# Kernel optimization log

Hardware: AMD Instinct MI355X
Metric: run time of the kernel (lower is better)

Reference implementation:

```python
import jax, jax.numpy as jnp
import numpy as np

EMB_DIM = 1024
B, K, N = 16, 512, 2048


def setup_inputs() -> dict:
    key0 = jax.random.key(0)
    k1, k2, k3, k4 = jax.random.split(key0, 4)
    query = jax.random.normal(k1, (K, EMB_DIM), dtype=jnp.float32)
    key = jax.random.normal(k2, (B, N, EMB_DIM), dtype=jnp.float32)
    # parameter W [emb_dim, emb_dim]; scale like kaiming-ish init
    W = jax.random.normal(k3, (EMB_DIM, EMB_DIM), dtype=jnp.float32) / np.sqrt(EMB_DIM)
    att_mask = jax.random.randint(k4, (B, K, N), 0, 2) > 0
    return {"query": query, "key": key, "W": W, "att_mask": att_mask}


def reference(query, key, W, att_mask):
    # 2D query / 3D key branch of SimpleConcatAttention, dim=-1
    d = query.shape[-1]
    # q @ W / sqrt(d): [K, d] (broadcast over batch instead of tiling)
    qW = (query @ W) / jnp.sqrt(jnp.asarray(d, query.dtype))
    # scores [b, K, N] = qW @ key^T
    att = jnp.einsum("kd,bnd->bkn", qW, key)
    att = jnp.where(att_mask, att, -jnp.inf)
    att = jax.nn.softmax(att, axis=-1)
    # out [b, K, d] = att @ key
    out = jnp.einsum("bkn,bnd->bkd", att, key)
    return out, att
```

## Files before the change

### kernel.cpp

```cpp
#include <hip/hip_runtime.h>


typedef float  f32x4  __attribute__((ext_vector_type(4)));
typedef short  bf16x8 __attribute__((ext_vector_type(8)));
typedef _Float16 f16x8 __attribute__((ext_vector_type(8)));
typedef unsigned short u16;
typedef unsigned short u16x8 __attribute__((ext_vector_type(8)));
typedef unsigned short u16x4 __attribute__((ext_vector_type(4)));

__device__ __forceinline__ void split2h(float x, u16& hi, u16& lo)
{
    _Float16 h = (_Float16)x;
    _Float16 l = (_Float16)(x - (float)h);
    hi = __builtin_bit_cast(u16, h);
    lo = __builtin_bit_cast(u16, l);
}

__device__ __forceinline__ void split2(float x, u16& hi, u16& lo)
{
    unsigned u = __float_as_uint(x);
    hi = (u16)(u >> 16);
    float hf = __uint_as_float(u & 0xFFFF0000u);
    float lf = x - hf;
    lo = (u16)(__float_as_uint(lf) >> 16);
}

__device__ __forceinline__ void async_cp16(const void* g, void* l)
{
    __builtin_amdgcn_global_load_lds(
        (const __attribute__((address_space(1))) unsigned int*)g,
        (__attribute__((address_space(3))) unsigned int*)l, 16, 0, 0);
}

template<int NMFMA, int BK>
__global__ __launch_bounds__(256, 2) void gemm_nt_f16(
    const u16* __restrict__ Ah, const u16* __restrict__ Al,
    const u16* __restrict__ Bh, const u16* __restrict__ Bl,
    float* __restrict__ C,
    int Kd, long sA, long sB, long sC, int ldc, float scale)
{
    constexpr int NPL = (NMFMA == 3) ? 4 : (NMFMA == 2) ? 3 : 2;
    constexpr int PS  = 128 * BK;
    constexpr int NCH = PS / 512;
    __shared__ __attribute__((aligned(16))) u16 lds[NPL * PS];
    u16* Ahs = lds;
    u16* Bhs = lds + PS;
    u16* Als = (NMFMA >= 2) ? lds + 2 * PS : nullptr;
    u16* Bls = (NMFMA == 3) ? lds + 3 * PS : nullptr;

    const int tid  = threadIdx.x;
    const int lane = tid & 63;
    const int wid  = tid >> 6;
    const int wm   = wid >> 1, wn = wid & 1;
    const int fr   = lane & 15;
    const int fq   = lane >> 4;

    const int m0 = blockIdx.y * 128, n0 = blockIdx.x * 128;
    const u16* Ag  = Ah + (long)blockIdx.z * sA + (long)m0 * Kd;
    const u16* Bg  = Bh + (long)blockIdx.z * sB + (long)n0 * Kd;
    const u16* Ag2 = (NMFMA >= 2) ? Al + (long)blockIdx.z * sA + (long)m0 * Kd : nullptr;
    const u16* Bg2 = (NMFMA == 3) ? Bl + (long)blockIdx.z * sB + (long)n0 * Kd : nullptr;

    f32x4 acc[4][4];
#pragma unroll
    for (int i = 0; i < 4; i++)
#pragma unroll
        for (int j = 0; j < 4; j++) acc[i][j] = (f32x4){0.f, 0.f, 0.f, 0.f};

    for (int k0 = 0; k0 < Kd; k0 += BK) {
        __syncthreads();
#pragma unroll
        for (int i = 0; i < NCH / 4; i++) {
            const int q   = wid * (NCH / 4) + i;
            const int p   = q * 512 + lane * 8;
            const int r   = p / BK;
            const int oct = (p & (BK - 1)) >> 3;
            const long go = (long)r * Kd + k0 + ((oct ^ (r & 7)) << 3);
            async_cp16(Ag + go, Ahs + q * 512);
            async_cp16(Bg + go, Bhs + q * 512);
            if constexpr (NMFMA >= 2) async_cp16(Ag2 + go, Als + q * 512);
            if constexpr (NMFMA == 3) async_cp16(Bg2 + go, Bls + q * 512);
        }
        __syncthreads();

#pragma unroll
        for (int ks = 0; ks < BK / 32; ks++) {
            const int cl = fq + ks * 4;
            f16x8 ah[4], bh[4], al[4], bl[4];
#pragma unroll
            for (int i = 0; i < 4; i++) {
                const int ra = wm * 64 + i * 16 + fr;
                const int oa = ra * BK + ((cl ^ (ra & 7)) << 3);
                ah[i] = *(const f16x8*)&Ahs[oa];
                if constexpr (NMFMA >= 2) al[i] = *(const f16x8*)&Als[oa];
                const int rb = wn * 64 + i * 16 + fr;
                const int ob = rb * BK + ((cl ^ (rb & 7)) << 3);
                bh[i] = *(const f16x8*)&Bhs[ob];
                if constexpr (NMFMA == 3) bl[i] = *(const f16x8*)&Bls[ob];
            }
#pragma unroll
            for (int i = 0; i < 4; i++)
#pragma unroll
                for (int j = 0; j < 4; j++) {
                    acc[i][j] = __builtin_amdgcn_mfma_f32_16x16x32_f16(ah[i], bh[j], acc[i][j], 0, 0, 0);
                    if constexpr (NMFMA == 3)
                        acc[i][j] = __builtin_amdgcn_mfma_f32_16x16x32_f16(ah[i], bl[j], acc[i][j], 0, 0, 0);
                    if constexpr (NMFMA >= 2)
                        acc[i][j] = __builtin_amdgcn_mfma_f32_16x16x32_f16(al[i], bh[j], acc[i][j], 0, 0, 0);
                }
        }
    }

    float* Cg = C + (long)blockIdx.z * sC + (long)(m0 + wm * 64) * ldc + (n0 + wn * 64);
    const int r4 = fq * 4;
#pragma unroll
    for (int i = 0; i < 4; i++)
#pragma unroll
        for (int j = 0; j < 4; j++) {
            float* cp = Cg + (long)(i * 16 + r4) * ldc + j * 16 + fr;
#pragma unroll
            for (int q = 0; q < 4; q++)
                cp[(long)q * ldc] = acc[i][j][q] * scale;
        }
}

__global__ __launch_bounds__(256) void prep_all(
    const float* __restrict__ query, const float* __restrict__ W,
    const float* __restrict__ key,
    u16* __restrict__ qW_h, u16* __restrict__ qW_l,
    u16* __restrict__ key_h, u16* __restrict__ keyT)
{
    constexpr int LDg = 72;
    __shared__ __attribute__((aligned(16))) u16 sm[4 * 64 * LDg];
    const int tid = threadIdx.x;

    if (blockIdx.x >= 128) {
        u16* t = sm;
        const int idx2 = (int)blockIdx.x - 128;
        const int bx = idx2 & 15, by = (idx2 >> 4) & 31, bz = idx2 >> 9;
        const long zin = (long)bz * 2048 * 1024;
        const int n0 = by * 64, d0 = bx * 64;
#pragma unroll
        for (int j = 0; j < 2; j++) {
            const int idx = tid + j * 256;
            const int row = idx >> 3;
            const int col = (idx & 7) * 8;
            const long g = zin + (long)(n0 + row) * 1024 + d0 + col;
            f32x4 v0 = *(const f32x4*)(key + g);
            f32x4 v1 = *(const f32x4*)(key + g + 4);
            u16x8 h;
#pragma unroll
            for (int e = 0; e < 4; e++) {
                _Float16 a = (_Float16)v0[e];
                _Float16 b = (_Float16)v1[e];
                h[e]     = __builtin_bit_cast(u16, a);
                h[4 + e] = __builtin_bit_cast(u16, b);
            }
            *(u16x8*)(key_h + g) = h;
#pragma unroll
            for (int e = 0; e < 8; e++) t[(col + e) * 65 + row] = h[e];
        }
        __syncthreads();
        const long zT = (long)bz * 1024 * 2048;
#pragma unroll
        for (int j = 0; j < 4; j++) {
            const int idx = tid + j * 256;
            const int dr = idx >> 4;
            const int nc = (idx & 15) * 4;
            u16x4 o = {t[dr * 65 + nc], t[dr * 65 + nc + 1],
                       t[dr * 65 + nc + 2], t[dr * 65 + nc + 3]};
            *(u16x4*)(keyT + zT + (long)(d0 + dr) * 2048 + n0 + nc) = o;
        }
        return;
    }

    u16* As_h = sm;
    u16* As_l = sm + 64 * LDg;
    u16* Bs_h = sm + 2 * 64 * LDg;
    u16* Bs_l = sm + 3 * 64 * LDg;

    const int lane = tid & 63, wid = tid >> 6;
    const int wm = wid >> 1, wn = wid & 1;
    const int lr = lane & 15, fq = lane >> 4;
    const int m0 = ((int)blockIdx.x >> 4) * 64;
    const int n0 = ((int)blockIdx.x & 15) * 64;
    const float* Ag = query + (long)m0 * 1024;
    const float* Bg = W + n0;

    __builtin_amdgcn_s_setprio(1);

    f32x4 acc[2][2];
#pragma unroll
    for (int i = 0; i < 2; i++)
#pragma unroll
        for (int j = 0; j < 2; j++) acc[i][j] = (f32x4){0.f, 0.f, 0.f, 0.f};

    for (int k0 = 0; k0 < 1024; k0 += 64) {
        __syncthreads();
        {
            const int row = tid >> 2, kb = (tid & 3) * 16;
            const float* src = Ag + (long)row * 1024 + k0 + kb;
            f32x4 v0 = *(const f32x4*)src;
            f32x4 v1 = *(const f32x4*)(src + 4);
            f32x4 v2 = *(const f32x4*)(src + 8);
            f32x4 v3 = *(const f32x4*)(src + 12);
            u16x8 h0, h1, l0, l1;
#pragma unroll
            for (int e = 0; e < 4; e++) {
                u16 hh, ll;
                split2h(v0[e], hh, ll); h0[e] = hh;     l0[e] = ll;
                split2h(v1[e], hh, ll); h0[4 + e] = hh; l0[4 + e] = ll;
                split2h(v2[e], hh, ll); h1[e] = hh;     l1[e] = ll;
                split2h(v3[e], hh, ll); h1[4 + e] = hh; l1[4 + e] = ll;
            }
            *(u16x8*)&As_h[row * LDg + kb]     = h0;
            *(u16x8*)&As_h[row * LDg + kb + 8] = h1;
            *(u16x8*)&As_l[row * LDg + kb]     = l0;
            *(u16x8*)&As_l[row * LDg + kb + 8] = l1;
        }
        {
            const int n = lane;
            u16x8 h0, h1, l0, l1;
#pragma unroll
            for (int kk = 0; kk < 8; kk++) {
                float x0 = Bg[(long)(k0 + wid * 16 + kk) * 1024 + n];
                float x1 = Bg[(long)(k0 + wid * 16 + 8 + kk) * 1024 + n];
                u16 hh, ll;
                split2h(x0, hh, ll); h0[kk] = hh; l0[kk] = ll;
                split2h(x1, hh, ll); h1[kk] = hh; l1[kk] = ll;
            }
            *(u16x8*)&Bs_h[n * LDg + wid * 16]     = h0;
            *(u16x8*)&Bs_h[n * LDg + wid * 16 + 8] = h1;
            *(u16x8*)&Bs_l[n * LDg + wid * 16]     = l0;
            *(u16x8*)&Bs_l[n * LDg + wid * 16 + 8] = l1;
        }
        __syncthreads();

#pragma unroll
        for (int ks = 0; ks < 2; ks++) {
            f16x8 ah[2], al[2], bh[2], bl[2];
#pragma unroll
            for (int i = 0; i < 2; i++) {
                const int ra = (wm * 32 + i * 16 + lr) * LDg + ks * 32 + fq * 8;
                ah[i] = *(const f16x8*)&As_h[ra];
                al[i] = *(const f16x8*)&As_l[ra];
                const int rb = (wn * 32 + i * 16 + lr) * LDg + ks * 32 + fq * 8;
                bh[i] = *(const f16x8*)&Bs_h[rb];
                bl[i] = *(const f16x8*)&Bs_l[rb];
            }
#pragma unroll
            for (int i = 0; i < 2; i++)
#pragma unroll
                for (int j = 0; j < 2; j++) {
                    acc[i][j] = __builtin_amdgcn_mfma_f32_16x16x32_f16(ah[i], bh[j], acc[i][j], 0, 0, 0);
                    acc[i][j] = __builtin_amdgcn_mfma_f32_16x16x32_f16(ah[i], bl[j], acc[i][j], 0, 0, 0);
                    acc[i][j] = __builtin_amdgcn_mfma_f32_16x16x32_f16(al[i], bh[j], acc[i][j], 0, 0, 0);
                }
        }
    }

    __builtin_amdgcn_s_setprio(0);

    const int r4 = fq * 4;
#pragma unroll
    for (int i = 0; i < 2; i++)
#pragma unroll
        for (int j = 0; j < 2; j++)
#pragma unroll
            for (int q = 0; q < 4; q++) {
                float v = acc[i][j][q] * (1.f / 32.f);
                u16 hh, ll;
                split2h(v, hh, ll);
                const long o = (long)(m0 + wm * 32 + i * 16 + r4 + q) * 1024
                             + n0 + wn * 32 + j * 16 + lr;
                qW_h[o] = hh;
                qW_l[o] = ll;
            }
}

template<bool BT>
__global__ __launch_bounds__(256, 2) void gemm_mfma(
    const float* __restrict__ A, const float* __restrict__ B,
    float* __restrict__ C,
    int Kd, int lda, int ldb, int ldc,
    long sA, long sB, long sC, float scale)
{
    constexpr int LD = 40;
    __shared__ __attribute__((aligned(16))) u16 As_hi[128 * LD];
    __shared__ __attribute__((aligned(16))) u16 As_lo[128 * LD];
    __shared__ __attribute__((aligned(16))) u16 Bs_hi[128 * LD];
    __shared__ __attribute__((aligned(16))) u16 Bs_lo[128 * LD];

    const int tid  = threadIdx.x;
    const int lane = tid & 63;
    const int wid  = tid >> 6;
    const int wm   = wid >> 1, wn = wid & 1;
    const int lr   = lane & 15;
    const int lk   = (lane >> 4) * 8;

    const int m0 = blockIdx.y * 128, n0 = blockIdx.x * 128;
    const float* Ag = A + (long)blockIdx.z * sA + (long)m0 * lda;
    const float* Bg = B + (long)blockIdx.z * sB + (BT ? (long)n0 * ldb : (long)n0);

    f32x4 acc[4][4];
#pragma unroll
    for (int i = 0; i < 4; i++)
#pragma unroll
        for (int j = 0; j < 4; j++) acc[i][j] = (f32x4){0.f, 0.f, 0.f, 0.f};

    for (int k0 = 0; k0 < Kd; k0 += 32) {
        __syncthreads();
#pragma unroll
        for (int it = 0; it < 2; it++) {
            const int p   = tid + it * 256;
            const int row = p >> 2, k8 = (p & 3) * 8;
            const float* src = Ag + (long)row * lda + k0 + k8;
            f32x4 v0 = *(const f32x4*)src;
            f32x4 v1 = *(const f32x4*)(src + 4);
            u16x8 h, l;
#pragma unroll
            for (int e = 0; e < 4; e++) {
                u16 hh, ll;
                split2(v0[e], hh, ll); h[e] = hh;     l[e] = ll;
                split2(v1[e], hh, ll); h[4 + e] = hh; l[4 + e] = ll;
            }
            *(u16x8*)&As_hi[row * LD + k8] = h;
            *(u16x8*)&As_lo[row * LD + k8] = l;
        }
        if constexpr (BT) {
#pragma unroll
            for (int it = 0; it < 2; it++) {
                const int p   = tid + it * 256;
                const int row = p >> 2, k8 = (p & 3) * 8;
                const float* src = Bg + (long)row * ldb + k0 + k8;
                f32x4 v0 = *(const f32x4*)src;
                f32x4 v1 = *(const f32x4*)(src + 4);
                u16x8 h, l;
#pragma unroll
                for (int e = 0; e < 4; e++) {
                    u16 hh, ll;
                    split2(v0[e], hh, ll); h[e] = hh;     l[e] = ll;
                    split2(v1[e], hh, ll); h[4 + e] = hh; l[4 + e] = ll;
                }
                *(u16x8*)&Bs_hi[row * LD + k8] = h;
                *(u16x8*)&Bs_lo[row * LD + k8] = l;
            }
        } else {
#pragma unroll
            for (int h2 = 0; h2 < 2; h2++) {
                const int n = h2 * 64 + lane;
                u16x8 h, l;
#pragma unroll
                for (int kk = 0; kk < 8; kk++) {
                    float x = Bg[(long)(k0 + wid * 8 + kk) * ldb + n];
                    u16 hh, ll;
                    split2(x, hh, ll);
                    h[kk] = hh; l[kk] = ll;
                }
                *(u16x8*)&Bs_hi[n * LD + wid * 8] = h;
                *(u16x8*)&Bs_lo[n * LD + wid * 8] = l;
            }
        }
        __syncthreads();

        bf16x8 ah[4], al[4], bh[4], bl[4];
#pragma unroll
        for (int i = 0; i < 4; i++) {
            const int ra = (wm * 64 + i * 16 + lr) * LD + lk;
            ah[i] = *(const bf16x8*)&As_hi[ra];
            al[i] = *(const bf16x8*)&As_lo[ra];
            const int rb = (wn * 64 + i * 16 + lr) * LD + lk;
            bh[i] = *(const bf16x8*)&Bs_hi[rb];
            bl[i] = *(const bf16x8*)&Bs_lo[rb];
        }
#pragma unroll
        for (int i = 0; i < 4; i++)
#pragma unroll
            for (int j = 0; j < 4; j++) {
                acc[i][j] = __builtin_amdgcn_mfma_f32_16x16x32_bf16(ah[i], bh[j], acc[i][j], 0, 0, 0);
                acc[i][j] = __builtin_amdgcn_mfma_f32_16x16x32_bf16(ah[i], bl[j], acc[i][j], 0, 0, 0);
                acc[i][j] = __builtin_amdgcn_mfma_f32_16x16x32_bf16(al[i], bh[j], acc[i][j], 0, 0, 0);
            }
    }

    float* Cg = C + (long)blockIdx.z * sC + (long)(m0 + wm * 64) * ldc + (n0 + wn * 64);
    const int r4 = (lane >> 4) * 4;
#pragma unroll
    for (int i = 0; i < 4; i++)
#pragma unroll
        for (int j = 0; j < 4; j++) {
            float* cp = Cg + (long)(i * 16 + r4) * ldc + j * 16 + lr;
#pragma unroll
            for (int q = 0; q < 4; q++)
                cp[(long)q * ldc] = acc[i][j][q] * scale;
        }
}

__global__ __launch_bounds__(256) void softmax_rows(
    float* __restrict__ att, const int* __restrict__ mask, u16* __restrict__ att_h)
{
    const int  row  = blockIdx.x;
    const int  tid  = threadIdx.x;
    const long base = (long)row * 2048 + tid * 8;

    f32x4 s0 = *(const f32x4*)(att + base);
    f32x4 s1 = *(const f32x4*)(att + base + 4);
    float x[8] = {s0[0], s0[1], s0[2], s0[3], s1[0], s1[1], s1[2], s1[3]};

    if (mask) {
        int4 mv0 = *(const int4*)(mask + base);
        int4 mv1 = *(const int4*)(mask + base + 4);
        const int mk[8] = {mv0.x, mv0.y, mv0.z, mv0.w, mv1.x, mv1.y, mv1.z, mv1.w};
#pragma unroll
        for (int j = 0; j < 8; j++) x[j] = mk[j] ? x[j] : -INFINITY;
    }

    float mx = x[0];
#pragma unroll
    for (int j = 1; j < 8; j++) mx = fmaxf(mx, x[j]);
#pragma unroll
    for (int off = 32; off > 0; off >>= 1) mx = fmaxf(mx, __shfl_down(mx, off));

    __shared__ float red[8];
    const int wave = tid >> 6, lane = tid & 63;
    if (lane == 0) red[wave] = mx;
    __syncthreads();
    mx = fmaxf(fmaxf(red[0], red[1]), fmaxf(red[2], red[3]));

    if (mx == -INFINITY) {
        f32x4 z = {0.f, 0.f, 0.f, 0.f};
        *(f32x4*)(att + base) = z;
        *(f32x4*)(att + base + 4) = z;
        if (att_h) {
            u16x8 zh = {0, 0, 0, 0, 0, 0, 0, 0};
            *(u16x8*)(att_h + base) = zh;
        }
        return;
    }

    float e[8], s = 0.f;
#pragma unroll
    for (int j = 0; j < 8; j++) { e[j] = __expf(x[j] - mx); s += e[j]; }
#pragma unroll
    for (int off = 32; off > 0; off >>= 1) s += __shfl_down(s, off);
    if (lane == 0) red[4 + wave] = s;
    __syncthreads();
    s = red[4] + red[5] + red[6] + red[7];

    const float inv = 1.f / s;
    f32x4 o0, o1;
#pragma unroll
    for (int j = 0; j < 4; j++) { o0[j] = e[j] * inv; o1[j] = e[4 + j] * inv; }
    *(f32x4*)(att + base) = o0;
    *(f32x4*)(att + base + 4) = o1;
    if (att_h) {
        u16x8 hv;
#pragma unroll
        for (int j = 0; j < 4; j++) {
            _Float16 h0 = (_Float16)o0[j];
            _Float16 h1 = (_Float16)o1[j];
            hv[j]     = __builtin_bit_cast(u16, h0);
            hv[4 + j] = __builtin_bit_cast(u16, h1);
        }
        *(u16x8*)(att_h + base) = hv;
    }
}

extern "C" void kernel_launch(void* const* d_in, const int* in_sizes, int n_in,
                              void* d_out, int out_size, void* d_ws, size_t ws_size,
                              hipStream_t stream)
{
    const float* query = nullptr;
    const float* key   = nullptr;
    const float* W     = nullptr;
    const int*   mask  = nullptr;
    for (int i = 0; i < n_in; i++) {
        switch (in_sizes[i]) {
            case 524288:   query = (const float*)d_in[i]; break;
            case 33554432: key   = (const float*)d_in[i]; break;
            case 1048576:  W     = (const float*)d_in[i]; break;
            case 16777216: mask  = (const int*)d_in[i];   break;
        }
    }

    float* out = (float*)d_out;
    float* att = out + (long)16 * 512 * 1024;

    const size_t NEED = (size_t)169869312;
    if (ws_size >= NEED) {
        char* w = (char*)d_ws;
        u16* key_h = (u16*)(w);
        u16* keyT  = (u16*)(w + 67108864);
        u16* att_h = (u16*)(w + 134217728);
        u16* qW_h  = (u16*)(w + 167772160);
        u16* qW_l  = (u16*)(w + 168820736);

        prep_all<<<dim3(128 + 8192), 256, 0, stream>>>(
            query, W, key, qW_h, qW_l, key_h, keyT);

        gemm_nt_f16<2, 64><<<dim3(16, 4, 16), 256, 0, stream>>>(
            qW_h, qW_l, key_h, nullptr, att,
            1024, 0L, (long)2048 * 1024, (long)512 * 2048, 2048, 1.f);

        softmax_rows<<<dim3(16 * 512), 256, 0, stream>>>(att, mask, att_h);

        gemm_nt_f16<1, 128><<<dim3(8, 4, 16), 256, 0, stream>>>(
            att_h, nullptr, keyT, nullptr, out,
            2048, (long)512 * 2048, (long)1024 * 2048, (long)512 * 1024, 1024, 1.f);
    } else {
        float* qW = out;
        gemm_mfma<false><<<dim3(8, 4, 1), 256, 0, stream>>>(
            query, W, qW, 1024, 1024, 1024, 1024, 0L, 0L, 0L, 1.f / 32.f);
        gemm_mfma<true><<<dim3(16, 4, 16), 256, 0, stream>>>(
            qW, key, att, 1024, 1024, 1024, 2048,
            0L, (long)2048 * 1024, (long)512 * 2048, 1.f);
        softmax_rows<<<dim3(16 * 512), 256, 0, stream>>>(att, mask, nullptr);
        gemm_mfma<false><<<dim3(8, 4, 16), 256, 0, stream>>>(
            att, key, out, 2048, 2048, 1024, 1024,
            (long)512 * 2048, (long)2048 * 1024, (long)512 * 1024, 1.f);
    }
}
```

Before: 217.8 us.

## Emit transposed fp16 key from first GEMM's LDS tiles instead of prep kernel

```diff
diff --git a/kernel.cpp b/kernel.cpp
--- a/kernel.cpp
+++ b/kernel.cpp
@@ -32,11 +32,11 @@
         (__attribute__((address_space(3))) unsigned int*)l, 16, 0, 0);
 }
 
-template<int NMFMA, int BK>
+template<int NMFMA, int BK, bool EMIT_BT>
 __global__ __launch_bounds__(256, 2) void gemm_nt_f16(
     const u16* __restrict__ Ah, const u16* __restrict__ Al,
     const u16* __restrict__ Bh, const u16* __restrict__ Bl,
-    float* __restrict__ C,
+    float* __restrict__ C, u16* __restrict__ KT,
     int Kd, long sA, long sB, long sC, int ldc, float scale)
 {
     constexpr int NPL = (NMFMA == 3) ? 4 : (NMFMA == 2) ? 3 : 2;
@@ -109,6 +109,26 @@
                         acc[i][j] = __builtin_amdgcn_mfma_f32_16x16x32_f16(al[i], bh[j], acc[i][j], 0, 0, 0);
                 }
         }
+
+        if constexpr (EMIT_BT) {
+            if (blockIdx.y == 0) {
+                u16* KTz = KT + (long)blockIdx.z * (long)Kd * 2048 + n0;
+#pragma unroll
+                for (int o = 0; o < 8; o++) {
+                    const int flat = tid + o * 256;
+                    const int d    = flat >> 5;
+                    const int nq   = (flat & 31) << 2;
+                    const int oct  = d >> 3, e = d & 7;
+                    u16x4 v;
+#pragma unroll
+                    for (int i = 0; i < 4; i++) {
+                        const int r = nq + i;
+                        v[i] = Bhs[r * BK + ((oct ^ (r & 7)) << 3) + e];
+                    }
+                    *(u16x4*)(KTz + (long)(k0 + d) * 2048 + nq) = v;
+                }
+            }
+        }
     }
 
     float* Cg = C + (long)blockIdx.z * sC + (long)(m0 + wm * 64) * ldc + (n0 + wn * 64);
@@ -128,49 +148,25 @@
     const float* __restrict__ query, const float* __restrict__ W,
     const float* __restrict__ key,
     u16* __restrict__ qW_h, u16* __restrict__ qW_l,
-    u16* __restrict__ key_h, u16* __restrict__ keyT)
+    u16* __restrict__ key_h)
 {
     constexpr int LDg = 72;
     __shared__ __attribute__((aligned(16))) u16 sm[4 * 64 * LDg];
     const int tid = threadIdx.x;
 
     if (blockIdx.x >= 128) {
-        u16* t = sm;
-        const int idx2 = (int)blockIdx.x - 128;
-        const int bx = idx2 & 15, by = (idx2 >> 4) & 31, bz = idx2 >> 9;
-        const long zin = (long)bz * 2048 * 1024;
-        const int n0 = by * 64, d0 = bx * 64;
-#pragma unroll
-        for (int j = 0; j < 2; j++) {
-            const int idx = tid + j * 256;
-            const int row = idx >> 3;
-            const int col = (idx & 7) * 8;
-            const long g = zin + (long)(n0 + row) * 1024 + d0 + col;
-            f32x4 v0 = *(const f32x4*)(key + g);
-            f32x4 v1 = *(const f32x4*)(key + g + 4);
-            u16x8 h;
-#pragma unroll
-            for (int e = 0; e < 4; e++) {
-                _Float16 a = (_Float16)v0[e];
-                _Float16 b = (_Float16)v1[e];
-                h[e]     = __builtin_bit_cast(u16, a);
-                h[4 + e] = __builtin_bit_cast(u16, b);
-            }
-            *(u16x8*)(key_h + g) = h;
-#pragma unroll
-            for (int e = 0; e < 8; e++) t[(col + e) * 65 + row] = h[e];
-        }
-        __syncthreads();
-        const long zT = (long)bz * 1024 * 2048;
-#pragma unroll
-        for (int j = 0; j < 4; j++) {
-            const int idx = tid + j * 256;
-            const int dr = idx >> 4;
-            const int nc = (idx & 15) * 4;
-            u16x4 o = {t[dr * 65 + nc], t[dr * 65 + nc + 1],
-                       t[dr * 65 + nc + 2], t[dr * 65 + nc + 3]};
-            *(u16x4*)(keyT + zT + (long)(d0 + dr) * 2048 + n0 + nc) = o;
-        }
+        const long base = ((long)blockIdx.x - 128) * 2048 + tid * 8;
+        f32x4 v0 = *(const f32x4*)(key + base);
+        f32x4 v1 = *(const f32x4*)(key + base + 4);
+        u16x8 h;
+#pragma unroll
+        for (int e = 0; e < 4; e++) {
+            _Float16 a = (_Float16)v0[e];
+            _Float16 b = (_Float16)v1[e];
+            h[e]     = __builtin_bit_cast(u16, a);
+            h[4 + e] = __builtin_bit_cast(u16, b);
+        }
+        *(u16x8*)(key_h + base) = h;
         return;
     }
 
@@ -495,17 +491,17 @@
         u16* qW_h  = (u16*)(w + 167772160);
         u16* qW_l  = (u16*)(w + 168820736);
 
-        prep_all<<<dim3(128 + 8192), 256, 0, stream>>>(
-            query, W, key, qW_h, qW_l, key_h, keyT);
-
-        gemm_nt_f16<2, 64><<<dim3(16, 4, 16), 256, 0, stream>>>(
-            qW_h, qW_l, key_h, nullptr, att,
+        prep_all<<<dim3(128 + 16384), 256, 0, stream>>>(
+            query, W, key, qW_h, qW_l, key_h);
+
+        gemm_nt_f16<2, 64, true><<<dim3(16, 4, 16), 256, 0, stream>>>(
+            qW_h, qW_l, key_h, nullptr, att, keyT,
             1024, 0L, (long)2048 * 1024, (long)512 * 2048, 2048, 1.f);
 
         softmax_rows<<<dim3(16 * 512), 256, 0, stream>>>(att, mask, att_h);
 
-        gemm_nt_f16<1, 128><<<dim3(8, 4, 16), 256, 0, stream>>>(
-            att_h, nullptr, keyT, nullptr, out,
+        gemm_nt_f16<1, 128, false><<<dim3(8, 4, 16), 256, 0, stream>>>(
+            att_h, nullptr, keyT, nullptr, out, nullptr,
             2048, (long)512 * 2048, (long)1024 * 2048, (long)512 * 1024, 1024, 1.f);
     } else {
         float* qW = out;
```

Result: slower. 282.8 us (+29.9%).

## Fuse fp32-to-fp16 key conversion into the score GEMM, drop key_h buffer

Applied to the files above, without the earlier changes.

```diff
diff --git a/kernel.cpp b/kernel.cpp
--- a/kernel.cpp
+++ b/kernel.cpp
@@ -32,21 +32,14 @@
         (__attribute__((address_space(3))) unsigned int*)l, 16, 0, 0);
 }
 
-template<int NMFMA, int BK>
-__global__ __launch_bounds__(256, 2) void gemm_nt_f16(
+__global__ __launch_bounds__(256, 2) void gemm_s(
     const u16* __restrict__ Ah, const u16* __restrict__ Al,
-    const u16* __restrict__ Bh, const u16* __restrict__ Bl,
-    float* __restrict__ C,
-    int Kd, long sA, long sB, long sC, int ldc, float scale)
-{
-    constexpr int NPL = (NMFMA == 3) ? 4 : (NMFMA == 2) ? 3 : 2;
-    constexpr int PS  = 128 * BK;
-    constexpr int NCH = PS / 512;
-    __shared__ __attribute__((aligned(16))) u16 lds[NPL * PS];
-    u16* Ahs = lds;
-    u16* Bhs = lds + PS;
-    u16* Als = (NMFMA >= 2) ? lds + 2 * PS : nullptr;
-    u16* Bls = (NMFMA == 3) ? lds + 3 * PS : nullptr;
+    const float* __restrict__ key, float* __restrict__ C)
+{
+    __shared__ __attribute__((aligned(16))) unsigned char smem[65536];
+    u16*   Ahs = (u16*)smem;
+    u16*   Als = (u16*)(smem + 16384);
+    float* Bfs = (float*)(smem + 32768);
 
     const int tid  = threadIdx.x;
     const int lane = tid & 63;
@@ -56,10 +49,9 @@
     const int fq   = lane >> 4;
 
     const int m0 = blockIdx.y * 128, n0 = blockIdx.x * 128;
-    const u16* Ag  = Ah + (long)blockIdx.z * sA + (long)m0 * Kd;
-    const u16* Bg  = Bh + (long)blockIdx.z * sB + (long)n0 * Kd;
-    const u16* Ag2 = (NMFMA >= 2) ? Al + (long)blockIdx.z * sA + (long)m0 * Kd : nullptr;
-    const u16* Bg2 = (NMFMA == 3) ? Bl + (long)blockIdx.z * sB + (long)n0 * Kd : nullptr;
+    const u16*   Ag  = Ah + (long)m0 * 1024;
+    const u16*   Ag2 = Al + (long)m0 * 1024;
+    const float* Bg  = key + (long)blockIdx.z * 2048 * 1024 + (long)n0 * 1024;
 
     f32x4 acc[4][4];
 #pragma unroll
@@ -67,47 +59,131 @@
 #pragma unroll
         for (int j = 0; j < 4; j++) acc[i][j] = (f32x4){0.f, 0.f, 0.f, 0.f};
 
+    for (int k0 = 0; k0 < 1024; k0 += 64) {
+        __syncthreads();
+#pragma unroll
+        for (int i = 0; i < 4; i++) {
+            const int q   = wid * 4 + i;
+            const int p   = q * 512 + lane * 8;
+            const int r   = p >> 6;
+            const int oct = (p & 63) >> 3;
+            const long go = (long)r * 1024 + k0 + ((oct ^ (r & 7)) << 3);
+            async_cp16(Ag + go, Ahs + q * 512);
+            async_cp16(Ag2 + go, Als + q * 512);
+        }
+#pragma unroll
+        for (int i = 0; i < 8; i++) {
+            const int q = wid * 8 + i;
+            const int G = q * 64 + lane;
+            const int r = G >> 4;
+            const int g = G & 15;
+            const long go = (long)r * 1024 + k0 + ((g ^ (r & 15)) << 2);
+            async_cp16(Bg + go, Bfs + q * 256);
+        }
+        __syncthreads();
+
+#pragma unroll
+        for (int ks = 0; ks < 2; ks++) {
+            const int cl = fq + ks * 4;
+            f16x8 ah[4], al[4], bh[4];
+#pragma unroll
+            for (int i = 0; i < 4; i++) {
+                const int ra = wm * 64 + i * 16 + fr;
+                const int oa = ra * 64 + ((cl ^ (ra & 7)) << 3);
+                ah[i] = *(const f16x8*)&Ahs[oa];
+                al[i] = *(const f16x8*)&Als[oa];
+                const int rb = wn * 64 + i * 16 + fr;
+                const int g0 = ((2 * cl)     ^ (rb & 15)) << 2;
+                const int g1 = ((2 * cl + 1) ^ (rb & 15)) << 2;
+                f32x4 b0 = *(const f32x4*)&Bfs[rb * 64 + g0];
+                f32x4 b1 = *(const f32x4*)&Bfs[rb * 64 + g1];
+#pragma unroll
+                for (int e = 0; e < 4; e++) {
+                    bh[i][e]     = (_Float16)b0[e];
+                    bh[i][4 + e] = (_Float16)b1[e];
+                }
+            }
+#pragma unroll
+            for (int i = 0; i < 4; i++)
+#pragma unroll
+                for (int j = 0; j < 4; j++) {
+                    acc[i][j] = __builtin_amdgcn_mfma_f32_16x16x32_f16(ah[i], bh[j], acc[i][j], 0, 0, 0);
+                    acc[i][j] = __builtin_amdgcn_mfma_f32_16x16x32_f16(al[i], bh[j], acc[i][j], 0, 0, 0);
+                }
+        }
+    }
+
+    float* Cg = C + (long)blockIdx.z * 512 * 2048 + (long)(m0 + wm * 64) * 2048 + (n0 + wn * 64);
+    const int r4 = fq * 4;
+#pragma unroll
+    for (int i = 0; i < 4; i++)
+#pragma unroll
+        for (int j = 0; j < 4; j++) {
+            float* cp = Cg + (long)(i * 16 + r4) * 2048 + j * 16 + fr;
+#pragma unroll
+            for (int q = 0; q < 4; q++)
+                cp[(long)q * 2048] = acc[i][j][q];
+        }
+}
+
+__global__ __launch_bounds__(256, 2) void gemm_nt_f16(
+    const u16* __restrict__ Ah, const u16* __restrict__ Bh,
+    float* __restrict__ C,
+    int Kd, long sA, long sB, long sC, int ldc)
+{
+    constexpr int BK = 128;
+    constexpr int PS = 128 * BK;
+    __shared__ __attribute__((aligned(16))) u16 lds[2 * PS];
+    u16* Ahs = lds;
+    u16* Bhs = lds + PS;
+
+    const int tid  = threadIdx.x;
+    const int lane = tid & 63;
+    const int wid  = tid >> 6;
+    const int wm   = wid >> 1, wn = wid & 1;
+    const int fr   = lane & 15;
+    const int fq   = lane >> 4;
+
+    const int m0 = blockIdx.y * 128, n0 = blockIdx.x * 128;
+    const u16* Ag = Ah + (long)blockIdx.z * sA + (long)m0 * Kd;
+    const u16* Bg = Bh + (long)blockIdx.z * sB + (long)n0 * Kd;
+
+    f32x4 acc[4][4];
+#pragma unroll
+    for (int i = 0; i < 4; i++)
+#pragma unroll
+        for (int j = 0; j < 4; j++) acc[i][j] = (f32x4){0.f, 0.f, 0.f, 0.f};
+
     for (int k0 = 0; k0 < Kd; k0 += BK) {
         __syncthreads();
 #pragma unroll
-        for (int i = 0; i < NCH / 4; i++) {
-            const int q   = wid * (NCH / 4) + i;
+        for (int i = 0; i < 8; i++) {
+            const int q   = wid * 8 + i;
             const int p   = q * 512 + lane * 8;
             const int r   = p / BK;
             const int oct = (p & (BK - 1)) >> 3;
             const long go = (long)r * Kd + k0 + ((oct ^ (r & 7)) << 3);
             async_cp16(Ag + go, Ahs + q * 512);
             async_cp16(Bg + go, Bhs + q * 512);
-            if constexpr (NMFMA >= 2) async_cp16(Ag2 + go, Als + q * 512);
-            if constexpr (NMFMA == 3) async_cp16(Bg2 + go, Bls + q * 512);
         }
         __syncthreads();
 
 #pragma unroll
         for (int ks = 0; ks < BK / 32; ks++) {
             const int cl = fq + ks * 4;
-            f16x8 ah[4], bh[4], al[4], bl[4];
+            f16x8 ah[4], bh[4];
 #pragma unroll
             for (int i = 0; i < 4; i++) {
                 const int ra = wm * 64 + i * 16 + fr;
-                const int oa = ra * BK + ((cl ^ (ra & 7)) << 3);
-                ah[i] = *(const f16x8*)&Ahs[oa];
-                if constexpr (NMFMA >= 2) al[i] = *(const f16x8*)&Als[oa];
+                ah[i] = *(const f16x8*)&Ahs[ra * BK + ((cl ^ (ra & 7)) << 3)];
                 const int rb = wn * 64 + i * 16 + fr;
-                const int ob = rb * BK + ((cl ^ (rb & 7)) << 3);
-                bh[i] = *(const f16x8*)&Bhs[ob];
-                if constexpr (NMFMA == 3) bl[i] = *(const f16x8*)&Bls[ob];
+                bh[i] = *(const f16x8*)&Bhs[rb * BK + ((cl ^ (rb & 7)) << 3)];
             }
 #pragma unroll
             for (int i = 0; i < 4; i++)
 #pragma unroll
-                for (int j = 0; j < 4; j++) {
+                for (int j = 0; j < 4; j++)
                     acc[i][j] = __builtin_amdgcn_mfma_f32_16x16x32_f16(ah[i], bh[j], acc[i][j], 0, 0, 0);
-                    if constexpr (NMFMA == 3)
-                        acc[i][j] = __builtin_amdgcn_mfma_f32_16x16x32_f16(ah[i], bl[j], acc[i][j], 0, 0, 0);
-                    if constexpr (NMFMA >= 2)
-                        acc[i][j] = __builtin_amdgcn_mfma_f32_16x16x32_f16(al[i], bh[j], acc[i][j], 0, 0, 0);
-                }
         }
     }
 
@@ -120,15 +196,14 @@
             float* cp = Cg + (long)(i * 16 + r4) * ldc + j * 16 + fr;
 #pragma unroll
             for (int q = 0; q < 4; q++)
-                cp[(long)q * ldc] = acc[i][j][q] * scale;
+                cp[(long)q * ldc] = acc[i][j][q];
         }
 }
 
 __global__ __launch_bounds__(256) void prep_all(
     const float* __restrict__ query, const float* __restrict__ W,
     const float* __restrict__ key,
-    u16* __restrict__ qW_h, u16* __restrict__ qW_l,
-    u16* __restrict__ key_h, u16* __restrict__ keyT)
+    u16* __restrict__ qW_h, u16* __restrict__ qW_l, u16* __restrict__ keyT)
 {
     constexpr int LDg = 72;
     __shared__ __attribute__((aligned(16))) u16 sm[4 * 64 * LDg];
@@ -141,24 +216,16 @@
         const long zin = (long)bz * 2048 * 1024;
         const int n0 = by * 64, d0 = bx * 64;
 #pragma unroll
-        for (int j = 0; j < 2; j++) {
+        for (int j = 0; j < 4; j++) {
             const int idx = tid + j * 256;
-            const int row = idx >> 3;
-            const int col = (idx & 7) * 8;
-            const long g = zin + (long)(n0 + row) * 1024 + d0 + col;
-            f32x4 v0 = *(const f32x4*)(key + g);
-            f32x4 v1 = *(const f32x4*)(key + g + 4);
-            u16x8 h;
+            const int row = idx >> 4;
+            const int col = (idx & 15) * 4;
+            f32x4 v = *(const f32x4*)(key + zin + (long)(n0 + row) * 1024 + d0 + col);
 #pragma unroll
             for (int e = 0; e < 4; e++) {
-                _Float16 a = (_Float16)v0[e];
-                _Float16 b = (_Float16)v1[e];
-                h[e]     = __builtin_bit_cast(u16, a);
-                h[4 + e] = __builtin_bit_cast(u16, b);
-            }
-            *(u16x8*)(key_h + g) = h;
-#pragma unroll
-            for (int e = 0; e < 8; e++) t[(col + e) * 65 + row] = h[e];
+                _Float16 hh = (_Float16)v[e];
+                t[(col + e) * 65 + row] = __builtin_bit_cast(u16, hh);
+            }
         }
         __syncthreads();
         const long zT = (long)bz * 1024 * 2048;
@@ -486,27 +553,24 @@
     float* out = (float*)d_out;
     float* att = out + (long)16 * 512 * 1024;
 
-    const size_t NEED = (size_t)169869312;
+    const size_t NEED = (size_t)102760448;
     if (ws_size >= NEED) {
         char* w = (char*)d_ws;
-        u16* key_h = (u16*)(w);
-        u16* keyT  = (u16*)(w + 67108864);
-        u16* att_h = (u16*)(w + 134217728);
-        u16* qW_h  = (u16*)(w + 167772160);
-        u16* qW_l  = (u16*)(w + 168820736);
+        u16* keyT  = (u16*)(w);
+        u16* att_h = (u16*)(w + 67108864);
+        u16* qW_h  = (u16*)(w + 100663296);
+        u16* qW_l  = (u16*)(w + 101711872);
 
         prep_all<<<dim3(128 + 8192), 256, 0, stream>>>(
-            query, W, key, qW_h, qW_l, key_h, keyT);
-
-        gemm_nt_f16<2, 64><<<dim3(16, 4, 16), 256, 0, stream>>>(
-            qW_h, qW_l, key_h, nullptr, att,
-            1024, 0L, (long)2048 * 1024, (long)512 * 2048, 2048, 1.f);
+            query, W, key, qW_h, qW_l, keyT);
+
+        gemm_s<<<dim3(16, 4, 16), 256, 0, stream>>>(qW_h, qW_l, key, att);
 
         softmax_rows<<<dim3(16 * 512), 256, 0, stream>>>(att, mask, att_h);
 
-        gemm_nt_f16<1, 128><<<dim3(8, 4, 16), 256, 0, stream>>>(
-            att_h, nullptr, keyT, nullptr, out,
-            2048, (long)512 * 2048, (long)1024 * 2048, (long)512 * 1024, 1024, 1.f);
+        gemm_nt_f16<<<dim3(8, 4, 16), 256, 0, stream>>>(
+            att_h, keyT, out,
+            2048, (long)512 * 2048, (long)1024 * 2048, (long)512 * 1024, 1024);
     } else {
         float* qW = out;
         gemm_mfma<false><<<dim3(8, 4, 1), 256, 0, stream>>>(
```

Measured after the change: 213.6 us. No clear change (-1.9%).
